# Performance work log

Hardware: AMD Instinct MI355X
Metric: run time of the kernel (lower is better)

## Reference

```python
import jax, jax.numpy as jnp
import numpy as np

H_HEADS = 8
HIDDEN = 512
D_K = HIDDEN // H_HEADS


def setup_inputs() -> dict:
    key = jax.random.key(0)
    ks = jax.random.split(key, 16)
    B, T = 4, 1024
    P = 2 * T - 1
    s = 0.02
    inp = {
        "x": jax.random.normal(ks[0], (B, T, HIDDEN), dtype=jnp.float32),
        "pos_emb": jax.random.normal(ks[1], (1, P, HIDDEN), dtype=jnp.float32),
        "Wq": jax.random.normal(ks[2], (HIDDEN, HIDDEN), dtype=jnp.float32) * s,
        "bq": jnp.zeros((HIDDEN,), dtype=jnp.float32),
        "Wk": jax.random.normal(ks[3], (HIDDEN, HIDDEN), dtype=jnp.float32) * s,
        "bk": jnp.zeros((HIDDEN,), dtype=jnp.float32),
        "Wv": jax.random.normal(ks[4], (HIDDEN, HIDDEN), dtype=jnp.float32) * s,
        "bv": jnp.zeros((HIDDEN,), dtype=jnp.float32),
        "Wp": jax.random.normal(ks[5], (HIDDEN, HIDDEN), dtype=jnp.float32) * s,
        "bp": jnp.zeros((HIDDEN,), dtype=jnp.float32),
        "Wo": jax.random.normal(ks[6], (HIDDEN, HIDDEN), dtype=jnp.float32) * s,
        "bo": jnp.zeros((HIDDEN,), dtype=jnp.float32),
        "pos_bias_u": jax.random.normal(ks[7], (H_HEADS, D_K), dtype=jnp.float32) * s,
        "pos_bias_v": jax.random.normal(ks[8], (H_HEADS, D_K), dtype=jnp.float32) * s,
    }
    return inp


def rel_shift(x):
    # x: (B, H, T, P). Transformer-XL relative shift.
    B, H, T, P = x.shape
    x = jnp.pad(x, ((0, 0), (0, 0), (0, 0), (1, 0)))  # (B,H,T,P+1)
    x = x.reshape(B, H, P + 1, T)[:, :, 1:, :]          # drop first row
    return x.reshape(B, H, T, P)


def reference(x, pos_emb, Wq, bq, Wk, bk, Wv, bv, Wp, bp, Wo, bo, pos_bias_u, pos_bias_v):
    B, T, _ = x.shape
    Hh, d = H_HEADS, D_K
    scale = 1.0 / jnp.sqrt(jnp.asarray(d, dtype=x.dtype))

    q = (x @ Wq + bq).reshape(B, T, Hh, d)                       # (B,T,H,d)
    k = (x @ Wk + bk).reshape(B, T, Hh, d).transpose(0, 2, 1, 3)  # (B,H,T,d)
    v = (x @ Wv + bv).reshape(B, T, Hh, d).transpose(0, 2, 1, 3)  # (B,H,T,d)
    P = pos_emb.shape[1]
    p = (pos_emb @ Wp + bp).reshape(pos_emb.shape[0], P, Hh, d).transpose(0, 2, 1, 3)  # (1,H,P,d)

    q_u = (q + pos_bias_u).transpose(0, 2, 1, 3)  # (B,H,T,d)
    q_v = (q + pos_bias_v).transpose(0, 2, 1, 3)  # (B,H,T,d)

    # content-position term with rel-shift (broadcast over batch dim of p)
    matrix_bd = jnp.matmul(q_v, p.transpose(0, 1, 3, 2))  # (B,H,T,P)
    matrix_bd = rel_shift(matrix_bd)[:, :, :, :T] * scale  # (B,H,T,T)

    # content-content term + additive bias, scaled softmax
    scores = jnp.matmul(q_u, k.transpose(0, 1, 3, 2)) * scale + matrix_bd
    attn = jax.nn.softmax(scores.astype(jnp.float32), axis=-1).astype(x.dtype)
    out = jnp.matmul(attn, v)                 # (B,H,T,d)
    out = out.transpose(0, 2, 1, 3).reshape(B, T, Hh * d)
    return out @ Wo + bo
```

## Files before the change

kernel.cpp:

```cpp
#include <hip/hip_runtime.h>
#include <math.h>

#define BATCH 4
#define SEQ   1024
#define HID   512
#define NHEAD 8

typedef unsigned short u16;
typedef unsigned int   u32;
typedef short  short8 __attribute__((ext_vector_type(8)));
typedef float  f32x4  __attribute__((ext_vector_type(4)));

__device__ __forceinline__ u16 f2bf(float x) {
  u32 u = __builtin_bit_cast(u32, x);
  u32 r = (u + 0x7FFFu + ((u >> 16) & 1u)) >> 16;
  return (u16)r;
}
__device__ __forceinline__ float bf2f(u16 h) {
  u32 u = ((u32)h) << 16;
  return __builtin_bit_cast(float, u);
}

#define DPPMAX(x, ctrl)                                                        \
  x = fmaxf(x, __builtin_bit_cast(float, __builtin_amdgcn_update_dpp(          \
                   0, __builtin_bit_cast(int, x), ctrl, 0xf, 0xf, true)))

__global__ __launch_bounds__(256)
void cvt_two(const float* __restrict__ x, const float* __restrict__ pe,
             u16* __restrict__ xb, u16* __restrict__ peb) {
  int i = blockIdx.x * 256 + threadIdx.x;
  const float* s;
  u16* d;
  if (i < 524288) {
    s = x; d = xb;
  } else {
    i -= 524288;
    if (i >= 262016) return;
    s = pe; d = peb;
  }
  float4 v = *(const float4*)&s[(size_t)i * 4];
  ushort4 o;
  o.x = f2bf(v.x); o.y = f2bf(v.y); o.z = f2bf(v.z); o.w = f2bf(v.w);
  *(ushort4*)&d[(size_t)i * 4] = o;
}

__global__ __launch_bounds__(256)
void transpose_w(const float* w0, const float* w1, const float* w2,
                 const float* w3, const float* w4, u16* __restrict__ wt) {
  const float* src;
  switch (blockIdx.z) {
    case 0: src = w0; break;
    case 1: src = w1; break;
    case 2: src = w2; break;
    case 3: src = w3; break;
    default: src = w4; break;
  }
  u16* dst = wt + (size_t)blockIdx.z * 512 * 512;
  __shared__ float t[32][33];
  const int tx = threadIdx.x, ty = threadIdx.y;
  const int k0 = blockIdx.x * 32, n0 = blockIdx.y * 32;
#pragma unroll
  for (int r = 0; r < 4; ++r)
    t[ty + 8 * r][tx] = src[(size_t)(k0 + ty + 8 * r) * 512 + n0 + tx];
  __syncthreads();
#pragma unroll
  for (int r = 0; r < 4; ++r)
    dst[(size_t)(n0 + ty + 8 * r) * 512 + k0 + tx] = f2bf(t[tx][ty + 8 * r]);
}

template <int MF, int NF>
__device__ __forceinline__ void gemm_core(const u16* __restrict__ A,
                                          const u16* __restrict__ Bt,
                                          int m0, int n0, u16* As, u16* Bs,
                                          f32x4 (&acc)[MF][NF]) {
  const int tid = threadIdx.x;
  const int wid = tid >> 6, lane = tid & 63;
  const int lr = lane & 15, lg = lane >> 4;
  const int wm = wid >> 1, wn = wid & 1;
  const int srow = tid >> 3, sc = tid & 7;
#pragma unroll
  for (int i = 0; i < MF; ++i)
#pragma unroll
    for (int j = 0; j < NF; ++j) acc[i][j] = (f32x4)0.f;

  for (int kt = 0; kt < 8; ++kt) {
    const int k0 = kt * 64;
    short8 la[MF], lb[NF];
#pragma unroll
    for (int r = 0; r < MF; ++r)
      la[r] = *(const short8*)&A[(size_t)(m0 + srow + 32 * r) * 512 + k0 + sc * 8];
#pragma unroll
    for (int r = 0; r < NF; ++r)
      lb[r] = *(const short8*)&Bt[(size_t)(n0 + srow + 32 * r) * 512 + k0 + sc * 8];
    __syncthreads();
#pragma unroll
    for (int r = 0; r < MF; ++r) {
      int row = srow + 32 * r;
      *(short8*)&As[row * 64 + ((sc ^ (row & 7)) * 8)] = la[r];
    }
#pragma unroll
    for (int r = 0; r < NF; ++r) {
      int row = srow + 32 * r;
      *(short8*)&Bs[row * 64 + ((sc ^ (row & 7)) * 8)] = lb[r];
    }
    __syncthreads();
#pragma unroll
    for (int kc = 0; kc < 2; ++kc) {
      const int ch = kc * 4 + lg;
      short8 af[MF], bfr[NF];
#pragma unroll
      for (int mt = 0; mt < MF; ++mt) {
        int row = wm * (MF * 16) + mt * 16 + lr;
        af[mt] = *(const short8*)&As[row * 64 + ((ch ^ (row & 7)) * 8)];
      }
#pragma unroll
      for (int nt = 0; nt < NF; ++nt) {
        int row = wn * (NF * 16) + nt * 16 + lr;
        bfr[nt] = *(const short8*)&Bs[row * 64 + ((ch ^ (row & 7)) * 8)];
      }
#pragma unroll
      for (int mt = 0; mt < MF; ++mt)
#pragma unroll
        for (int nt = 0; nt < NF; ++nt)
          acc[mt][nt] = __builtin_amdgcn_mfma_f32_16x16x32_bf16(
              af[mt], bfr[nt], acc[mt][nt], 0, 0, 0);
    }
  }
}

__global__ __launch_bounds__(256)
void gemm_qkvp(const u16* __restrict__ xbf, const u16* __restrict__ pebf,
               const u16* __restrict__ wt,
               const float* __restrict__ bq, const float* __restrict__ bk,
               const float* __restrict__ bv, const float* __restrict__ bp,
               const float* __restrict__ pbu, const float* __restrict__ pbv,
               u16* __restrict__ qu, u16* __restrict__ qv,
               u16* __restrict__ kk, u16* __restrict__ vt,
               u16* __restrict__ pp) {
  __shared__ __align__(16) u16 As[128 * 64];
  __shared__ __align__(16) u16 Bs[128 * 64];
  const int z = blockIdx.z;
  if (z == 3 && blockIdx.y >= 16) return;
  const u16* A = (z == 3) ? pebf : xbf;
  const u16* Bt = wt + (size_t)z * 512 * 512;
  const float* bias = (z == 0) ? bq : (z == 1) ? bk : (z == 2) ? bv : bp;
  const int m0 = blockIdx.y * 128, n0 = blockIdx.x * 128;

  f32x4 acc[4][4];
  gemm_core<4, 4>(A, Bt, m0, n0, As, Bs, acc);

  const int tid = threadIdx.x, wid = tid >> 6, lane = tid & 63;
  const int lr = lane & 15, lg = lane >> 4, wm = wid >> 1, wn = wid & 1;
#pragma unroll
  for (int mt = 0; mt < 4; ++mt)
#pragma unroll
    for (int nt = 0; nt < 4; ++nt) {
      const int col = n0 + wn * 64 + nt * 16 + lr;
      const int rb = m0 + wm * 64 + mt * 16 + lg * 4;
      const float bcol = bias[col];
      if (z == 0) {
        const float uu = pbu[col], vv = pbv[col];
#pragma unroll
        for (int q = 0; q < 4; ++q) {
          float val = acc[mt][nt][q] + bcol;
          qu[(size_t)(rb + q) * 512 + col] = f2bf(val + uu);
          qv[(size_t)(rb + q) * 512 + col] = f2bf(val + vv);
        }
      } else if (z == 1) {
#pragma unroll
        for (int q = 0; q < 4; ++q)
          kk[(size_t)(rb + q) * 512 + col] = f2bf(acc[mt][nt][q] + bcol);
      } else if (z == 2) {
        ushort4 pk;
        pk.x = f2bf(acc[mt][nt][0] + bcol);
        pk.y = f2bf(acc[mt][nt][1] + bcol);
        pk.z = f2bf(acc[mt][nt][2] + bcol);
        pk.w = f2bf(acc[mt][nt][3] + bcol);
        int bb = rb >> 10, tl = rb & 1023;
        *(ushort4*)&vt[(size_t)((bb * 8 + (col >> 6)) * 64 + (col & 63)) * 1024 + tl] = pk;
      } else {
#pragma unroll
        for (int q = 0; q < 4; ++q)
          if (rb + q < 2047)
            pp[(size_t)(rb + q) * 512 + col] = f2bf(acc[mt][nt][q] + bcol);
      }
    }
}

__global__ __launch_bounds__(256)
void gemm_wo(const u16* __restrict__ ao, const u16* __restrict__ wt,
             const float* __restrict__ bo, float* __restrict__ out) {
  __shared__ __align__(16) u16 As[64 * 64];
  __shared__ __align__(16) u16 Bs[64 * 64];
  const int m0 = blockIdx.y * 64, n0 = blockIdx.x * 64;
  f32x4 acc[2][2];
  gemm_core<2, 2>(ao, wt + (size_t)4 * 512 * 512, m0, n0, As, Bs, acc);
  const int tid = threadIdx.x, wid = tid >> 6, lane = tid & 63;
  const int lr = lane & 15, lg = lane >> 4, wm = wid >> 1, wn = wid & 1;
#pragma unroll
  for (int mt = 0; mt < 2; ++mt)
#pragma unroll
    for (int nt = 0; nt < 2; ++nt) {
      const int col = n0 + wn * 32 + nt * 16 + lr;
      const int rb = m0 + wm * 32 + mt * 16 + lg * 4;
      const float bcol = bo[col];
#pragma unroll
      for (int q = 0; q < 4; ++q)
        out[(size_t)(rb + q) * 512 + col] = acc[mt][nt][q] + bcol;
    }
}

__global__ __launch_bounds__(256)
void attn_mfma(const u16* __restrict__ quP, const u16* __restrict__ qvP,
               const u16* __restrict__ kP, const u16* __restrict__ vtP,
               const u16* __restrict__ pP, u16* __restrict__ ao) {
  __shared__ __align__(16) u16 Ks[64 * 64];
  __shared__ __align__(16) u16 Vs[64 * 64];
  __shared__ __align__(16) u16 Ps[128 * 64];
  __shared__ __align__(16) u16 Es[4][16 * 64];
  __shared__ float Bds[4][16][84];

  const int tid = threadIdx.x;
  const int wid = tid >> 6, lane = tid & 63;
  const int lr = lane & 15, lg = lane >> 4;
  const int srow = tid >> 3, sc = tid & 7;
  const int t0 = blockIdx.x * 64, h = blockIdx.y, b = blockIdx.z;

  short8 aqu[2], aqv[2];
#pragma unroll
  for (int kc = 0; kc < 2; ++kc) {
    size_t g = (size_t)(b * SEQ + t0 + wid * 16 + lr) * 512 + h * 64 + kc * 32 + lg * 8;
    aqu[kc] = *(const short8*)&quP[g];
    aqv[kc] = *(const short8*)&qvP[g];
  }
  short8 ones;
#pragma unroll
  for (int i = 0; i < 8; ++i) ones[i] = (short)0x3F80;

  float mrun[4] = {-1e30f, -1e30f, -1e30f, -1e30f};
  f32x4 cL = (f32x4)0.f;
  f32x4 cO[4];
#pragma unroll
  for (int i = 0; i < 4; ++i) cO[i] = (f32x4)0.f;

  u16* esw = &Es[wid][0];

  for (int j0 = 0; j0 < SEQ; j0 += 64) {
    const int base = 960 - t0 + j0;
    short8 lk[2], lv[2], lp[4];
#pragma unroll
    for (int r = 0; r < 2; ++r) {
      int row = srow + 32 * r;
      lk[r] = *(const short8*)&kP[(size_t)(b * SEQ + j0 + row) * 512 + h * 64 + sc * 8];
      lv[r] = *(const short8*)&vtP[(size_t)((b * 8 + h) * 64 + row) * 1024 + j0 + sc * 8];
    }
#pragma unroll
    for (int r = 0; r < 4; ++r) {
      int row = srow + 32 * r;
      lp[r] = *(const short8*)&pP[(size_t)(base + row) * 512 + h * 64 + sc * 8];
    }
    __syncthreads();
#pragma unroll
    for (int r = 0; r < 2; ++r) {
      int row = srow + 32 * r;
      *(short8*)&Ks[row * 64 + ((sc ^ (row & 7)) * 8)] = lk[r];
      *(short8*)&Vs[row * 64 + ((sc ^ (row & 7)) * 8)] = lv[r];
    }
#pragma unroll
    for (int r = 0; r < 4; ++r) {
      int row = srow + 32 * r;
      *(short8*)&Ps[row * 64 + ((sc ^ (row & 7)) * 8)] = lp[r];
    }
    __syncthreads();

    f32x4 cK[4], cP5[5];
#pragma unroll
    for (int i = 0; i < 4; ++i) cK[i] = (f32x4)0.f;
#pragma unroll
    for (int i = 0; i < 5; ++i) cP5[i] = (f32x4)0.f;
    __builtin_amdgcn_s_setprio(1);
#pragma unroll
    for (int kc = 0; kc < 2; ++kc) {
      const int ch = kc * 4 + lg;
#pragma unroll
      for (int nt = 0; nt < 4; ++nt) {
        int row = nt * 16 + lr;
        short8 bk = *(const short8*)&Ks[row * 64 + ((ch ^ (row & 7)) * 8)];
        cK[nt] = __builtin_amdgcn_mfma_f32_16x16x32_bf16(aqu[kc], bk, cK[nt], 0, 0, 0);
      }
#pragma unroll
      for (int pt = 0; pt < 5; ++pt) {
        int row = (3 - wid + pt) * 16 + lr;
        short8 bp = *(const short8*)&Ps[row * 64 + ((ch ^ (row & 7)) * 8)];
        cP5[pt] = __builtin_amdgcn_mfma_f32_16x16x32_bf16(aqv[kc], bp, cP5[pt], 0, 0, 0);
      }
    }
    __builtin_amdgcn_s_setprio(0);

#pragma unroll
    for (int pt = 0; pt < 5; ++pt)
#pragma unroll
      for (int q = 0; q < 4; ++q)
        Bds[wid][lg * 4 + q][pt * 16 + lr] = cP5[pt][q];
    float s[4][4];
#pragma unroll
    for (int q = 0; q < 4; ++q) {
      const int m = lg * 4 + q;
#pragma unroll
      for (int nt = 0; nt < 4; ++nt)
        s[nt][q] = 0.125f * (cK[nt][q] + Bds[wid][m][15 - m + nt * 16 + lr]);
    }

    float pm[4];
#pragma unroll
    for (int q = 0; q < 4; ++q) {
      float tm = fmaxf(fmaxf(s[0][q], s[1][q]), fmaxf(s[2][q], s[3][q]));
      DPPMAX(tm, 0xB1);
      DPPMAX(tm, 0x4E);
      DPPMAX(tm, 0x141);
      DPPMAX(tm, 0x140);
      pm[q] = tm;
    }
    int need = 0;
#pragma unroll
    for (int q = 0; q < 4; ++q) need |= (pm[q] > mrun[q] + 8.f) ? 1 : 0;
    if (__any(need)) {
#pragma unroll
      for (int q = 0; q < 4; ++q) {
        float mnew = fmaxf(mrun[q], pm[q]);
        float corr = __expf(mrun[q] - mnew);
        mrun[q] = mnew;
        cL[q] *= corr;
#pragma unroll
        for (int nt = 0; nt < 4; ++nt) cO[nt][q] *= corr;
      }
    }

#pragma unroll
    for (int nt = 0; nt < 4; ++nt) {
      int jp = nt * 16 + lr, sw = jp >> 3, jb = jp & 7;
#pragma unroll
      for (int q = 0; q < 4; ++q) {
        int m = lg * 4 + q;
        esw[m * 64 + ((sw ^ (m & 7)) * 8) + jb] = f2bf(__expf(s[nt][q] - mrun[q]));
      }
    }

    __builtin_amdgcn_s_setprio(1);
#pragma unroll
    for (int kc = 0; kc < 2; ++kc) {
      const int ch = kc * 4 + lg;
      short8 ae = *(const short8*)&esw[lr * 64 + ((ch ^ (lr & 7)) * 8)];
      cL = __builtin_amdgcn_mfma_f32_16x16x32_bf16(ae, ones, cL, 0, 0, 0);
#pragma unroll
      for (int nt = 0; nt < 4; ++nt) {
        int vr = nt * 16 + lr;
        short8 bv = *(const short8*)&Vs[vr * 64 + ((ch ^ (vr & 7)) * 8)];
        cO[nt] = __builtin_amdgcn_mfma_f32_16x16x32_bf16(ae, bv, cO[nt], 0, 0, 0);
      }
    }
    __builtin_amdgcn_s_setprio(0);
    __syncthreads();
  }

  float inv[4];
#pragma unroll
  for (int q = 0; q < 4; ++q) inv[q] = 1.f / cL[q];
#pragma unroll
  for (int nt = 0; nt < 4; ++nt)
#pragma unroll
    for (int q = 0; q < 4; ++q) {
      int row = b * SEQ + t0 + wid * 16 + lg * 4 + q;
      ao[(size_t)row * 512 + h * 64 + nt * 16 + lr] = f2bf(cO[nt][q] * inv[q]);
    }
}

extern "C" void kernel_launch(void* const* d_in, const int* in_sizes, int n_in,
                              void* d_out, int out_size, void* d_ws, size_t ws_size,
                              hipStream_t stream) {
  const float* x   = (const float*)d_in[0];
  const float* pe  = (const float*)d_in[1];
  const float* Wq  = (const float*)d_in[2];
  const float* bq  = (const float*)d_in[3];
  const float* Wk  = (const float*)d_in[4];
  const float* bk  = (const float*)d_in[5];
  const float* Wv  = (const float*)d_in[6];
  const float* bv  = (const float*)d_in[7];
  const float* Wp  = (const float*)d_in[8];
  const float* bp  = (const float*)d_in[9];
  const float* Wo  = (const float*)d_in[10];
  const float* bo  = (const float*)d_in[11];
  const float* pbu = (const float*)d_in[12];
  const float* pbv = (const float*)d_in[13];

  char* ws = (char*)d_ws;
  size_t o = 0;
  auto alloc = [&](size_t bytes) { size_t r = o; o += (bytes + 255) & ~(size_t)255; return r; };
  u16* x_bf  = (u16*)(ws + alloc((size_t)4096 * 512 * 2));
  u16* pe_bf = (u16*)(ws + alloc((size_t)2048 * 512 * 2));
  u16* wt    = (u16*)(ws + alloc((size_t)5 * 512 * 512 * 2));
  u16* qu    = (u16*)(ws + alloc((size_t)4096 * 512 * 2));
  u16* qv    = (u16*)(ws + alloc((size_t)4096 * 512 * 2));
  u16* kk    = (u16*)(ws + alloc((size_t)4096 * 512 * 2));
  u16* vt    = (u16*)(ws + alloc((size_t)4096 * 512 * 2));
  u16* pp    = (u16*)(ws + alloc((size_t)2048 * 512 * 2));
  u16* ao    = (u16*)(ws + alloc((size_t)4096 * 512 * 2));

  dim3 blk(256);
  cvt_two<<<dim3(3072), blk, 0, stream>>>(x, pe, x_bf, pe_bf);
  transpose_w<<<dim3(16, 16, 5), dim3(32, 8), 0, stream>>>(Wq, Wk, Wv, Wp, Wo, wt);
  hipMemsetAsync(pp + (size_t)2047 * 512, 0, 512 * 2, stream);

  gemm_qkvp<<<dim3(4, 32, 4), blk, 0, stream>>>(x_bf, pe_bf, wt, bq, bk, bv, bp,
                                                pbu, pbv, qu, qv, kk, vt, pp);
  attn_mfma<<<dim3(16, NHEAD, BATCH), blk, 0, stream>>>(qu, qv, kk, vt, pp, ao);
  gemm_wo<<<dim3(8, 64), blk, 0, stream>>>(ao, wt, bo, (float*)d_out);
}
```

Before: 86.16 us.

## Split attention key range across wave groups with prefetch and ring-buffered positions

Restructures the attention kernel so two wave groups each process alternate 64-key halves of a 128-key step. Each wave handles 32 query rows and shares every K fragment across two MFMAs. Next-step K/V/P tiles are prefetched into registers during compute, and position rows go into a 192-row ring buffer so overlapping position tiles are reused instead of reloaded. The two groups' partial softmax states are merged through shared memory at the end. This halves the loop trip count and the barrier count, at the cost of more registers, extra LDS, and a final reduction step.

```diff
diff --git a/kernel.cpp b/kernel.cpp
--- a/kernel.cpp
+++ b/kernel.cpp
@@ -15,10 +15,6 @@
   u32 u = __builtin_bit_cast(u32, x);
   u32 r = (u + 0x7FFFu + ((u >> 16) & 1u)) >> 16;
   return (u16)r;
-}
-__device__ __forceinline__ float bf2f(u16 h) {
-  u32 u = ((u32)h) << 16;
-  return __builtin_bit_cast(float, u);
 }
 
 #define DPPMAX(x, ctrl)                                                        \
@@ -214,165 +210,253 @@
 void attn_mfma(const u16* __restrict__ quP, const u16* __restrict__ qvP,
                const u16* __restrict__ kP, const u16* __restrict__ vtP,
                const u16* __restrict__ pP, u16* __restrict__ ao) {
-  __shared__ __align__(16) u16 Ks[64 * 64];
-  __shared__ __align__(16) u16 Vs[64 * 64];
-  __shared__ __align__(16) u16 Ps[128 * 64];
-  __shared__ __align__(16) u16 Es[4][16 * 64];
-  __shared__ float Bds[4][16][84];
+  __shared__ __align__(16) u16 Ks[2][4096];
+  __shared__ __align__(16) u16 Vs[2][4096];
+  __shared__ __align__(16) u16 Ps[192 * 64];
+  __shared__ __align__(16) float Wb[4][1504];
 
   const int tid = threadIdx.x;
   const int wid = tid >> 6, lane = tid & 63;
   const int lr = lane & 15, lg = lane >> 4;
-  const int srow = tid >> 3, sc = tid & 7;
+  const int grp = wid >> 1, wq = wid & 1;
   const int t0 = blockIdx.x * 64, h = blockIdx.y, b = blockIdx.z;
-
-  short8 aqu[2], aqv[2];
-#pragma unroll
-  for (int kc = 0; kc < 2; ++kc) {
-    size_t g = (size_t)(b * SEQ + t0 + wid * 16 + lr) * 512 + h * 64 + kc * 32 + lg * 8;
-    aqu[kc] = *(const short8*)&quP[g];
-    aqv[kc] = *(const short8*)&qvP[g];
-  }
+  const int base0 = 960 - t0;
+
+  float* wb = &Wb[wid][0];
+  u16* esw = (u16*)wb;
+
+  short8 aqu[2][2], aqv[2][2];
+#pragma unroll
+  for (int f = 0; f < 2; ++f)
+#pragma unroll
+    for (int kc = 0; kc < 2; ++kc) {
+      size_t g = (size_t)(b * SEQ + t0 + 32 * wq + 16 * f + lr) * 512 + h * 64 +
+                 kc * 32 + lg * 8;
+      aqu[f][kc] = *(const short8*)&quP[g];
+      aqv[f][kc] = *(const short8*)&qvP[g];
+    }
   short8 ones;
 #pragma unroll
   for (int i = 0; i < 8; ++i) ones[i] = (short)0x3F80;
 
-  float mrun[4] = {-1e30f, -1e30f, -1e30f, -1e30f};
-  f32x4 cL = (f32x4)0.f;
-  f32x4 cO[4];
-#pragma unroll
-  for (int i = 0; i < 4; ++i) cO[i] = (f32x4)0.f;
-
-  u16* esw = &Es[wid][0];
-
-  for (int j0 = 0; j0 < SEQ; j0 += 64) {
-    const int base = 960 - t0 + j0;
-    short8 lk[2], lv[2], lp[4];
-#pragma unroll
-    for (int r = 0; r < 2; ++r) {
-      int row = srow + 32 * r;
-      lk[r] = *(const short8*)&kP[(size_t)(b * SEQ + j0 + row) * 512 + h * 64 + sc * 8];
-      lv[r] = *(const short8*)&vtP[(size_t)((b * 8 + h) * 64 + row) * 1024 + j0 + sc * 8];
-    }
-#pragma unroll
-    for (int r = 0; r < 4; ++r) {
-      int row = srow + 32 * r;
-      lp[r] = *(const short8*)&pP[(size_t)(base + row) * 512 + h * 64 + sc * 8];
-    }
-    __syncthreads();
-#pragma unroll
-    for (int r = 0; r < 2; ++r) {
-      int row = srow + 32 * r;
-      *(short8*)&Ks[row * 64 + ((sc ^ (row & 7)) * 8)] = lk[r];
-      *(short8*)&Vs[row * 64 + ((sc ^ (row & 7)) * 8)] = lv[r];
-    }
-#pragma unroll
-    for (int r = 0; r < 4; ++r) {
-      int row = srow + 32 * r;
-      *(short8*)&Ps[row * 64 + ((sc ^ (row & 7)) * 8)] = lp[r];
-    }
-    __syncthreads();
-
-    f32x4 cK[4], cP5[5];
-#pragma unroll
-    for (int i = 0; i < 4; ++i) cK[i] = (f32x4)0.f;
-#pragma unroll
-    for (int i = 0; i < 5; ++i) cP5[i] = (f32x4)0.f;
+  float mrun[2][4];
+  f32x4 cL[2], cO[2][4];
+#pragma unroll
+  for (int f = 0; f < 2; ++f) {
+    cL[f] = (f32x4)0.f;
+#pragma unroll
+    for (int q = 0; q < 4; ++q) mrun[f][q] = -1e30f;
+#pragma unroll
+    for (int nt = 0; nt < 4; ++nt) cO[f][nt] = (f32x4)0.f;
+  }
+
+#pragma unroll
+  for (int r = 0; r < 4; ++r) {
+    int idx = tid + 256 * r;
+    int row = idx >> 3, sc = idx & 7;
+    short8 lk = *(const short8*)&kP[(size_t)(b * SEQ + row) * 512 + h * 64 + sc * 8];
+    short8 lv = *(const short8*)&vtP[(size_t)((b * 8 + h) * 64 + (row & 63)) * 1024 +
+                                     (row >> 6) * 64 + sc * 8];
+    *(short8*)&Ks[row >> 6][(row & 63) * 64 + ((sc ^ (row & 7)) * 8)] = lk;
+    *(short8*)&Vs[row >> 6][(row & 63) * 64 + ((sc ^ (row & 7)) * 8)] = lv;
+  }
+#pragma unroll
+  for (int r = 0; r < 6; ++r) {
+    int idx = tid + 256 * r;
+    int prow = idx >> 3, sc = idx & 7;
+    short8 lp = *(const short8*)&pP[(size_t)(base0 + prow) * 512 + h * 64 + sc * 8];
+    *(short8*)&Ps[prow * 64 + ((sc ^ (prow & 7)) * 8)] = lp;
+  }
+  __syncthreads();
+
+  int jb_self = 64 * grp;
+  int jbs = 0;
+
+  for (int s = 0; s < 8; ++s) {
+    short8 nk[4], nv[4], np[4];
+    if (s < 7) {
+      const int jn = 128 * (s + 1);
+#pragma unroll
+      for (int r = 0; r < 4; ++r) {
+        int idx = tid + 256 * r;
+        int row = idx >> 3, sc = idx & 7;
+        nk[r] = *(const short8*)&kP[(size_t)(b * SEQ + jn + row) * 512 + h * 64 + sc * 8];
+        nv[r] = *(const short8*)&vtP[(size_t)((b * 8 + h) * 64 + (row & 63)) * 1024 +
+                                     jn + (row >> 6) * 64 + sc * 8];
+        np[r] = *(const short8*)&pP[(size_t)(1152 - t0 + 128 * s + row) * 512 +
+                                    h * 64 + sc * 8];
+      }
+    }
+
+    f32x4 cK[2][4];
+#pragma unroll
+    for (int f = 0; f < 2; ++f)
+#pragma unroll
+      for (int nt = 0; nt < 4; ++nt) cK[f][nt] = (f32x4)0.f;
     __builtin_amdgcn_s_setprio(1);
 #pragma unroll
     for (int kc = 0; kc < 2; ++kc) {
       const int ch = kc * 4 + lg;
 #pragma unroll
       for (int nt = 0; nt < 4; ++nt) {
-        int row = nt * 16 + lr;
-        short8 bk = *(const short8*)&Ks[row * 64 + ((ch ^ (row & 7)) * 8)];
-        cK[nt] = __builtin_amdgcn_mfma_f32_16x16x32_bf16(aqu[kc], bk, cK[nt], 0, 0, 0);
-      }
-#pragma unroll
-      for (int pt = 0; pt < 5; ++pt) {
-        int row = (3 - wid + pt) * 16 + lr;
-        short8 bp = *(const short8*)&Ps[row * 64 + ((ch ^ (row & 7)) * 8)];
-        cP5[pt] = __builtin_amdgcn_mfma_f32_16x16x32_bf16(aqv[kc], bp, cP5[pt], 0, 0, 0);
+        int krow = nt * 16 + lr;
+        short8 bk = *(const short8*)&Ks[grp][krow * 64 + ((ch ^ (krow & 7)) * 8)];
+        cK[0][nt] = __builtin_amdgcn_mfma_f32_16x16x32_bf16(aqu[0][kc], bk, cK[0][nt], 0, 0, 0);
+        cK[1][nt] = __builtin_amdgcn_mfma_f32_16x16x32_bf16(aqu[1][kc], bk, cK[1][nt], 0, 0, 0);
       }
     }
     __builtin_amdgcn_s_setprio(0);
 
 #pragma unroll
-    for (int pt = 0; pt < 5; ++pt)
-#pragma unroll
-      for (int q = 0; q < 4; ++q)
-        Bds[wid][lg * 4 + q][pt * 16 + lr] = cP5[pt][q];
-    float s[4][4];
-#pragma unroll
-    for (int q = 0; q < 4; ++q) {
-      const int m = lg * 4 + q;
+    for (int f = 0; f < 2; ++f) {
+      const int gg = 2 * wq + f;
+      f32x4 cP5[5];
+#pragma unroll
+      for (int i = 0; i < 5; ++i) cP5[i] = (f32x4)0.f;
+      __builtin_amdgcn_s_setprio(1);
+#pragma unroll
+      for (int kc = 0; kc < 2; ++kc) {
+        const int ch = kc * 4 + lg;
+        const int swz = (ch ^ (lr & 7)) * 8;
+#pragma unroll
+        for (int pt = 0; pt < 5; ++pt) {
+          int pr = jb_self + (3 - gg + pt) * 16 + lr;
+          if (pr >= 192) pr -= 192;
+          short8 bp = *(const short8*)&Ps[pr * 64 + swz];
+          cP5[pt] = __builtin_amdgcn_mfma_f32_16x16x32_bf16(aqv[f][kc], bp, cP5[pt], 0, 0, 0);
+        }
+      }
+      __builtin_amdgcn_s_setprio(0);
+
+#pragma unroll
+      for (int pt = 0; pt < 5; ++pt)
+#pragma unroll
+        for (int q = 0; q < 4; ++q)
+          wb[(lg * 4 + q) * 94 + pt * 16 + lr + lg * 4] = cP5[pt][q];
+      float sv[4][4];
 #pragma unroll
       for (int nt = 0; nt < 4; ++nt)
-        s[nt][q] = 0.125f * (cK[nt][q] + Bds[wid][m][15 - m + nt * 16 + lr]);
-    }
-
-    float pm[4];
-#pragma unroll
-    for (int q = 0; q < 4; ++q) {
-      float tm = fmaxf(fmaxf(s[0][q], s[1][q]), fmaxf(s[2][q], s[3][q]));
-      DPPMAX(tm, 0xB1);
-      DPPMAX(tm, 0x4E);
-      DPPMAX(tm, 0x141);
-      DPPMAX(tm, 0x140);
-      pm[q] = tm;
-    }
-    int need = 0;
-#pragma unroll
-    for (int q = 0; q < 4; ++q) need |= (pm[q] > mrun[q] + 8.f) ? 1 : 0;
-    if (__any(need)) {
+#pragma unroll
+        for (int q = 0; q < 4; ++q)
+          sv[nt][q] = 0.125f * (cK[f][nt][q] +
+                                wb[(lg * 4 + q) * 94 + 15 - q + nt * 16 + lr]);
+
+      float pm[4];
 #pragma unroll
       for (int q = 0; q < 4; ++q) {
-        float mnew = fmaxf(mrun[q], pm[q]);
-        float corr = __expf(mrun[q] - mnew);
-        mrun[q] = mnew;
-        cL[q] *= corr;
-#pragma unroll
-        for (int nt = 0; nt < 4; ++nt) cO[nt][q] *= corr;
-      }
-    }
-
-#pragma unroll
-    for (int nt = 0; nt < 4; ++nt) {
-      int jp = nt * 16 + lr, sw = jp >> 3, jb = jp & 7;
+        float tm = fmaxf(fmaxf(sv[0][q], sv[1][q]), fmaxf(sv[2][q], sv[3][q]));
+        DPPMAX(tm, 0xB1);
+        DPPMAX(tm, 0x4E);
+        DPPMAX(tm, 0x141);
+        DPPMAX(tm, 0x140);
+        pm[q] = tm;
+      }
+      int need = 0;
+#pragma unroll
+      for (int q = 0; q < 4; ++q) need |= (pm[q] > mrun[f][q] + 8.f) ? 1 : 0;
+      if (__any(need)) {
+#pragma unroll
+        for (int q = 0; q < 4; ++q) {
+          float mnew = fmaxf(mrun[f][q], pm[q]);
+          float corr = __expf(mrun[f][q] - mnew);
+          mrun[f][q] = mnew;
+          cL[f][q] *= corr;
+#pragma unroll
+          for (int nt = 0; nt < 4; ++nt) cO[f][nt][q] *= corr;
+        }
+      }
+
+#pragma unroll
+      for (int nt = 0; nt < 4; ++nt) {
+        int jp = nt * 16 + lr, sw = jp >> 3, jb8 = jp & 7;
+#pragma unroll
+        for (int q = 0; q < 4; ++q) {
+          int m = lg * 4 + q;
+          esw[m * 64 + ((sw ^ (m & 7)) * 8) + jb8] = f2bf(__expf(sv[nt][q] - mrun[f][q]));
+        }
+      }
+
+      __builtin_amdgcn_s_setprio(1);
+#pragma unroll
+      for (int kc = 0; kc < 2; ++kc) {
+        const int ch = kc * 4 + lg;
+        short8 ae = *(const short8*)&esw[lr * 64 + ((ch ^ (lr & 7)) * 8)];
+        cL[f] = __builtin_amdgcn_mfma_f32_16x16x32_bf16(ae, ones, cL[f], 0, 0, 0);
+#pragma unroll
+        for (int nt = 0; nt < 4; ++nt) {
+          int vr = nt * 16 + lr;
+          short8 bv = *(const short8*)&Vs[grp][vr * 64 + ((ch ^ (vr & 7)) * 8)];
+          cO[f][nt] = __builtin_amdgcn_mfma_f32_16x16x32_bf16(ae, bv, cO[f][nt], 0, 0, 0);
+        }
+      }
+      __builtin_amdgcn_s_setprio(0);
+    }
+
+    __syncthreads();
+    if (s < 7) {
+#pragma unroll
+      for (int r = 0; r < 4; ++r) {
+        int idx = tid + 256 * r;
+        int row = idx >> 3, sc = idx & 7;
+        *(short8*)&Ks[row >> 6][(row & 63) * 64 + ((sc ^ (row & 7)) * 8)] = nk[r];
+        *(short8*)&Vs[row >> 6][(row & 63) * 64 + ((sc ^ (row & 7)) * 8)] = nv[r];
+        int pph = jbs + row;
+        if (pph >= 192) pph -= 192;
+        *(short8*)&Ps[pph * 64 + ((sc ^ (row & 7)) * 8)] = np[r];
+      }
+    }
+    jbs += 128; if (jbs >= 192) jbs -= 192;
+    jb_self += 128; if (jb_self >= 192) jb_self -= 192;
+    __syncthreads();
+  }
+
+  float* ob = (float*)&Ks[0][0];
+  float* mlb = (float*)&Vs[0][0];
+  if (grp == 1) {
+#pragma unroll
+    for (int f = 0; f < 2; ++f)
+#pragma unroll
+      for (int nt = 0; nt < 4; ++nt)
+#pragma unroll
+        for (int q = 0; q < 4; ++q)
+          ob[(wq * 32 + 16 * f + 4 * lg + q) * 64 + nt * 16 + lr] = cO[f][nt][q];
+    if (lr == 0) {
+#pragma unroll
+      for (int f = 0; f < 2; ++f)
+#pragma unroll
+        for (int q = 0; q < 4; ++q) {
+          int rr = wq * 32 + 16 * f + 4 * lg + q;
+          mlb[rr * 2 + 0] = mrun[f][q];
+          mlb[rr * 2 + 1] = cL[f][q];
+        }
+    }
+  }
+  __syncthreads();
+  if (grp == 0) {
+#pragma unroll
+    for (int f = 0; f < 2; ++f) {
+      float ws0[4], ws1[4];
 #pragma unroll
       for (int q = 0; q < 4; ++q) {
-        int m = lg * 4 + q;
-        esw[m * 64 + ((sw ^ (m & 7)) * 8) + jb] = f2bf(__expf(s[nt][q] - mrun[q]));
-      }
-    }
-
-    __builtin_amdgcn_s_setprio(1);
-#pragma unroll
-    for (int kc = 0; kc < 2; ++kc) {
-      const int ch = kc * 4 + lg;
-      short8 ae = *(const short8*)&esw[lr * 64 + ((ch ^ (lr & 7)) * 8)];
-      cL = __builtin_amdgcn_mfma_f32_16x16x32_bf16(ae, ones, cL, 0, 0, 0);
-#pragma unroll
-      for (int nt = 0; nt < 4; ++nt) {
-        int vr = nt * 16 + lr;
-        short8 bv = *(const short8*)&Vs[vr * 64 + ((ch ^ (vr & 7)) * 8)];
-        cO[nt] = __builtin_amdgcn_mfma_f32_16x16x32_bf16(ae, bv, cO[nt], 0, 0, 0);
-      }
-    }
-    __builtin_amdgcn_s_setprio(0);
-    __syncthreads();
-  }
-
-  float inv[4];
-#pragma unroll
-  for (int q = 0; q < 4; ++q) inv[q] = 1.f / cL[q];
-#pragma unroll
-  for (int nt = 0; nt < 4; ++nt)
-#pragma unroll
-    for (int q = 0; q < 4; ++q) {
-      int row = b * SEQ + t0 + wid * 16 + lg * 4 + q;
-      ao[(size_t)row * 512 + h * 64 + nt * 16 + lr] = f2bf(cO[nt][q] * inv[q]);
-    }
+        int rr = wq * 32 + 16 * f + 4 * lg + q;
+        float m1 = mlb[rr * 2 + 0], l1 = mlb[rr * 2 + 1];
+        float M = fmaxf(mrun[f][q], m1);
+        float w0 = __expf(mrun[f][q] - M), w1 = __expf(m1 - M);
+        float inv = 1.f / (w0 * cL[f][q] + w1 * l1);
+        ws0[q] = w0 * inv;
+        ws1[q] = w1 * inv;
+      }
+#pragma unroll
+      for (int nt = 0; nt < 4; ++nt)
+#pragma unroll
+        for (int q = 0; q < 4; ++q) {
+          int rr = wq * 32 + 16 * f + 4 * lg + q;
+          float o1 = ob[rr * 64 + nt * 16 + lr];
+          float val = ws0[q] * cO[f][nt][q] + ws1[q] * o1;
+          ao[(size_t)(b * SEQ + t0 + rr) * 512 + h * 64 + nt * 16 + lr] = f2bf(val);
+        }
+    }
+  }
 }
 
 extern "C" void kernel_launch(void* const* d_in, const int* in_sizes, int n_in,
```

After: 110.0 us. +27.7%, slower.
